# Performance work log

Measured on AMD Instinct MI355X. Metric: run time of the kernel, lower is better.

## Reference

```python
import jax, jax.numpy as jnp
import numpy as np

B, S, DIM = 2, 2048, 1024
H, W = 16, 256
HD = DIM // H
SCALE = HD ** -0.5


def setup_inputs() -> dict:
    key = jax.random.key(0)
    ks = jax.random.split(key, 9)
    std = DIM ** -0.5
    return {
        "x": jax.random.normal(ks[0], (B, S, DIM), dtype=jnp.float32),
        "Wq": jax.random.normal(ks[1], (DIM, DIM), dtype=jnp.float32) * std,
        "bq": jnp.zeros((DIM,), dtype=jnp.float32),
        "Wk": jax.random.normal(ks[2], (DIM, DIM), dtype=jnp.float32) * std,
        "bk": jnp.zeros((DIM,), dtype=jnp.float32),
        "Wv": jax.random.normal(ks[3], (DIM, DIM), dtype=jnp.float32) * std,
        "bv": jnp.zeros((DIM,), dtype=jnp.float32),
        "Wo": jax.random.normal(ks[4], (DIM, DIM), dtype=jnp.float32) * std,
        "bo": jnp.zeros((DIM,), dtype=jnp.float32),
    }


def reference(x, Wq, bq, Wk, bk, Wv, bv, Wo, bo):
    b, s, dim = x.shape
    q = (x @ Wq + bq).reshape(b, s, H, HD).transpose(0, 2, 1, 3)  # [B,H,S,HD]
    k = (x @ Wk + bk).reshape(b, s, H, HD).transpose(0, 2, 1, 3)
    v = (x @ Wv + bv).reshape(b, s, H, HD).transpose(0, 2, 1, 3)

    scores = jnp.einsum("bhid,bhjd->bhij", q, k) * SCALE  # [B,H,S,S]
    i = jnp.arange(s)[:, None]
    j = jnp.arange(s)[None, :]
    # valid keys: within causal sliding window [i-W+1, i]
    valid = (j <= i) & (j >= i - W + 1)
    scores = jnp.where(valid, scores, -jnp.inf)
    attn = jax.nn.softmax(scores, axis=-1)
    out = jnp.einsum("bhij,bhjd->bhid", attn, v)  # [B,H,S,HD]
    out = out.transpose(0, 2, 1, 3).reshape(b, s, dim)
    return out @ Wo + bo
```

## Files before the change

### kernel.cpp

```cpp
#include <hip/hip_runtime.h>
#include <stdint.h>

typedef __bf16 bf16;
typedef __bf16 bf16x8 __attribute__((ext_vector_type(8)));
typedef float f32x4 __attribute__((ext_vector_type(4)));

#define MFMA16(a, b, c) __builtin_amdgcn_mfma_f32_16x16x32_bf16((a), (b), (c), 0, 0, 0)

__device__ __forceinline__ void ldsdma16(const void* g, void* l) {
  __builtin_amdgcn_global_load_lds((const __attribute__((address_space(1))) void*)g,
                                   (__attribute__((address_space(3))) void*)l, 16, 0, 0);
}

__global__ __launch_bounds__(256) void prep_kernel(const float* __restrict__ x,
                                                   const float* __restrict__ Wq,
                                                   const float* __restrict__ Wk,
                                                   const float* __restrict__ Wv,
                                                   const float* __restrict__ Wo,
                                                   bf16* __restrict__ xb,
                                                   bf16* __restrict__ WT) {
  __shared__ float tile[64][65];
  if (blockIdx.z == 4) {
    const int t = (blockIdx.y * 16 + blockIdx.x) * 256 + threadIdx.x;
#pragma unroll
    for (int i = 0; i < 16; ++i) {
      const int idx = (t + i * 65536) * 4;
      float4 v = *(const float4*)(x + idx);
      union { bf16 h[4]; uint2 u; } p;
      p.h[0] = (bf16)v.x; p.h[1] = (bf16)v.y; p.h[2] = (bf16)v.z; p.h[3] = (bf16)v.w;
      *(uint2*)(xb + idx) = p.u;
    }
    return;
  }
  const float* src = blockIdx.z == 0 ? Wq : blockIdx.z == 1 ? Wk : blockIdx.z == 2 ? Wv : Wo;
  bf16* dst = WT + (size_t)blockIdx.z * 1024 * 1024;
  const int k0 = blockIdx.y * 64, n0 = blockIdx.x * 64;
  const int rr = threadIdx.x >> 6, c = threadIdx.x & 63;
#pragma unroll
  for (int i = 0; i < 16; ++i) {
    int r = i * 4 + rr;
    tile[r][c] = src[(size_t)(k0 + r) * 1024 + n0 + c];
  }
  __syncthreads();
#pragma unroll
  for (int i = 0; i < 16; ++i) {
    int r = i * 4 + rr;
    dst[(size_t)(n0 + r) * 1024 + k0 + c] = (bf16)tile[c][r];
  }
}

template <int NJ>
__device__ __forceinline__ void gemm_mainloop(const bf16* __restrict__ A,
                                              const bf16* __restrict__ BT, int K,
                                              int m0, int n0, bf16* As, bf16* Bs,
                                              f32x4 (&acc)[4][NJ]) {
  constexpr int BN = NJ * 32;
  const int tid = threadIdx.x;
  const int lane = tid & 63;
  const int wave = tid >> 6;
  const int wm = wave >> 1, wn = wave & 1;
  const int quad = lane >> 4, l16 = lane & 15;

  const f32x4 zero = {0.f, 0.f, 0.f, 0.f};
#pragma unroll
  for (int i = 0; i < 4; ++i)
#pragma unroll
    for (int j = 0; j < NJ; ++j) acc[i][j] = zero;

  for (int k0 = 0; k0 < K; k0 += 32) {
#pragma unroll
    for (int c = 0; c < 2; ++c) {
      int chunk = wave * 128 + c * 64 + lane;
      int row = chunk >> 2;
      int cg = (chunk & 3) ^ ((row >> 1) & 3);
      ldsdma16(A + (size_t)(m0 + row) * K + k0 + cg * 8,
               (char*)As + (size_t)(wave * 128 + c * 64) * 16);
    }
#pragma unroll
    for (int c = 0; c < BN / 64; ++c) {
      int chunk = wave * (BN / 64) * 64 + c * 64 + lane;
      int row = chunk >> 2;
      int cg = (chunk & 3) ^ ((row >> 1) & 3);
      ldsdma16(BT + (size_t)(n0 + row) * K + k0 + cg * 8,
               (char*)Bs + (size_t)(wave * (BN / 64) * 64 + c * 64) * 16);
    }
    __syncthreads();
    bf16x8 af[4], bfv[NJ];
#pragma unroll
    for (int i = 0; i < 4; ++i) {
      int ra = wm * 64 + i * 16 + l16;
      af[i] = ((const bf16x8*)As)[ra * 4 + (quad ^ ((ra >> 1) & 3))];
    }
#pragma unroll
    for (int j = 0; j < NJ; ++j) {
      int rb = wn * (BN / 2) + j * 16 + l16;
      bfv[j] = ((const bf16x8*)Bs)[rb * 4 + (quad ^ ((rb >> 1) & 3))];
    }
#pragma unroll
    for (int i = 0; i < 4; ++i)
#pragma unroll
      for (int j = 0; j < NJ; ++j) acc[i][j] = MFMA16(af[i], bfv[j], acc[i][j]);
    __syncthreads();
  }
}

__global__ __launch_bounds__(256) void qkv_gemm(const bf16* __restrict__ xb,
                                                const bf16* __restrict__ WT,
                                                const float* __restrict__ bq,
                                                const float* __restrict__ bk,
                                                const float* __restrict__ bv,
                                                bf16* __restrict__ Qd,
                                                bf16* __restrict__ Kd,
                                                bf16* __restrict__ Vd) {
  __shared__ bf16 As[128 * 32] __attribute__((aligned(16)));
  __shared__ bf16 Bs[128 * 32] __attribute__((aligned(16)));
  f32x4 acc[4][4];
  const int m0 = blockIdx.y * 128, n0 = blockIdx.x * 128;
  gemm_mainloop<4>(xb, WT, 1024, m0, n0, As, Bs, acc);

  const int lane = threadIdx.x & 63, wave = threadIdx.x >> 6;
  const int wm = wave >> 1, wn = wave & 1;
  const int quad = lane >> 4, l16 = lane & 15;
#pragma unroll
  for (int j = 0; j < 4; ++j) {
    const int n = n0 + wn * 64 + j * 16 + l16;
    const int sel = n >> 10, d = n & 1023;
    const float bias = (sel == 0 ? bq : sel == 1 ? bk : bv)[d];
    bf16* dst = (sel == 0 ? Qd : sel == 1 ? Kd : Vd);
    const float scl = (sel == 0) ? 0.125f : 1.f;
    const int h = d >> 6, hd = d & 63;
#pragma unroll
    for (int i = 0; i < 4; ++i) {
#pragma unroll
      for (int r = 0; r < 4; ++r) {
        const int token = m0 + wm * 64 + i * 16 + quad * 4 + r;
        const int bb = token >> 11, s = token & 2047;
        const float v = (acc[i][j][r] + bias) * scl;
        dst[((((size_t)bb * 16 + h) * 2048 + s) << 6) + hd] = (bf16)v;
      }
    }
  }
}

template <int NT, int MODE>
__device__ __forceinline__ void attn_phase(const int start, const bf16* __restrict__ Kb,
                                           const bf16* __restrict__ Vb, bf16* Ks, bf16* Vt,
                                           bf16* Psw, const bf16x8 qa0, const bf16x8 qa1,
                                           const int i0, float (&mrow)[4], float (&lrow)[4],
                                           f32x4 (&oacc)[4]) {
  const int tid = threadIdx.x, lane = tid & 63, wave = tid >> 6;
  const int quad = lane >> 4, l16 = lane & 15;
  const f32x4 zero = {0.f, 0.f, 0.f, 0.f};

  __syncthreads();
#pragma unroll
  for (int c = 0; c < NT / 2; ++c) {
    int chunk = c * 256 + wave * 64 + lane;
    int row = chunk >> 3;
    int cg = (chunk & 7) ^ (row & 7);
    ldsdma16(Kb + (size_t)(start + row) * 64 + cg * 8,
             (char*)Ks + (size_t)(c * 256 + wave * 64) * 16);
  }
  if (NT == 8) {
    const int key = tid >> 1, hc = (tid & 1) * 32;
    const bf16* vp = Vb + (size_t)(start + key) * 64 + hc;
    bf16x8 v0 = ((const bf16x8*)vp)[0], v1 = ((const bf16x8*)vp)[1];
    bf16x8 v2 = ((const bf16x8*)vp)[2], v3 = ((const bf16x8*)vp)[3];
#pragma unroll
    for (int i = 0; i < 8; ++i) Vt[(hc + i) * 136 + key] = v0[i];
#pragma unroll
    for (int i = 0; i < 8; ++i) Vt[(hc + 8 + i) * 136 + key] = v1[i];
#pragma unroll
    for (int i = 0; i < 8; ++i) Vt[(hc + 16 + i) * 136 + key] = v2[i];
#pragma unroll
    for (int i = 0; i < 8; ++i) Vt[(hc + 24 + i) * 136 + key] = v3[i];
  } else {
    const int key = tid >> 2, hc = (tid & 3) * 16;
    const bf16* vp = Vb + (size_t)(start + key) * 64 + hc;
    bf16x8 v0 = ((const bf16x8*)vp)[0], v1 = ((const bf16x8*)vp)[1];
#pragma unroll
    for (int i = 0; i < 8; ++i) Vt[(hc + i) * 136 + key] = v0[i];
#pragma unroll
    for (int i = 0; i < 8; ++i) Vt[(hc + 8 + i) * 136 + key] = v1[i];
  }
  __syncthreads();

  f32x4 sc[NT];
  __builtin_amdgcn_s_setprio(1);
#pragma unroll
  for (int nt = 0; nt < NT; ++nt) {
    int key = nt * 16 + l16;
    bf16x8 kb0 = ((const bf16x8*)Ks)[key * 8 + ((0 * 4 + quad) ^ (key & 7))];
    bf16x8 kb1 = ((const bf16x8*)Ks)[key * 8 + ((1 * 4 + quad) ^ (key & 7))];
    f32x4 s = zero;
    s = MFMA16(qa0, kb0, s);
    s = MFMA16(qa1, kb1, s);
    sc[nt] = s;
  }
  __builtin_amdgcn_s_setprio(0);

  float alpha[4];
#pragma unroll
  for (int r = 0; r < 4; ++r) {
    const int i = i0 + r;
    float mx = -1e30f;
#pragma unroll
    for (int nt = 0; nt < NT; ++nt) {
      float s = sc[nt][r];
      if (MODE == 1) {
        const bool valid = (start + nt * 16 + l16 + 255 >= i);
        s = valid ? s : -1e30f;
        sc[nt][r] = s;
      } else if (MODE == 2) {
        const bool valid = (start + nt * 16 + l16 <= i);
        s = valid ? s : -1e30f;
        sc[nt][r] = s;
      }
      mx = fmaxf(mx, s);
    }
#pragma unroll
    for (int m = 8; m >= 1; m >>= 1) mx = fmaxf(mx, __shfl_xor(mx, m, 64));
    const float mnew = fmaxf(mrow[r], mx);
    alpha[r] = __expf(mrow[r] - mnew);
    mrow[r] = mnew;
    float rs = 0.f;
#pragma unroll
    for (int nt = 0; nt < NT; ++nt) {
      const float p = __expf(sc[nt][r] - mnew);
      sc[nt][r] = p;
      rs += p;
    }
#pragma unroll
    for (int m = 8; m >= 1; m >>= 1) rs += __shfl_xor(rs, m, 64);
    lrow[r] = lrow[r] * alpha[r] + rs;
  }

#pragma unroll
  for (int nt = 0; nt < NT; ++nt)
#pragma unroll
    for (int r = 0; r < 4; ++r)
      Psw[(quad * 4 + r) * 136 + nt * 16 + l16] = (bf16)sc[nt][r];
  asm volatile("s_waitcnt lgkmcnt(0)" ::: "memory");
  bf16x8 pa[NT / 2];
#pragma unroll
  for (int ks = 0; ks < NT / 2; ++ks)
    pa[ks] = ((const bf16x8*)Psw)[l16 * 17 + ks * 4 + quad];

  __builtin_amdgcn_s_setprio(1);
#pragma unroll
  for (int ht = 0; ht < 4; ++ht) {
    f32x4 o = oacc[ht];
#pragma unroll
    for (int r = 0; r < 4; ++r) o[r] *= alpha[r];
#pragma unroll
    for (int ks = 0; ks < NT / 2; ++ks) {
      bf16x8 vb = ((const bf16x8*)Vt)[(ht * 16 + l16) * 17 + ks * 4 + quad];
      o = MFMA16(pa[ks], vb, o);
    }
    oacc[ht] = o;
  }
  __builtin_amdgcn_s_setprio(0);
}

__global__ __launch_bounds__(256) void attn_kernel(const bf16* __restrict__ Q,
                                                   const bf16* __restrict__ K,
                                                   const bf16* __restrict__ V,
                                                   bf16* __restrict__ Ao) {
  __shared__ bf16 Ks[128 * 64] __attribute__((aligned(16)));
  __shared__ bf16 Vt[64 * 136] __attribute__((aligned(16)));
  __shared__ bf16 Ps[4][16 * 136] __attribute__((aligned(16)));

  const int tid = threadIdx.x, lane = tid & 63, wave = tid >> 6;
  const int quad = lane >> 4, l16 = lane & 15;
  const int qt = blockIdx.x, h = blockIdx.y, b = blockIdx.z;
  const int q0 = qt * 64;
  const size_t base = ((size_t)(b * 16 + h)) * 2048 * 64;
  const bf16* Qb = Q + base + (size_t)q0 * 64;
  const bf16* Kb = K + base;
  const bf16* Vb = V + base;

  const bf16* qrow = Qb + (size_t)(wave * 16 + l16) * 64 + quad * 8;
  const bf16x8 qa0 = *(const bf16x8*)qrow;
  const bf16x8 qa1 = *(const bf16x8*)(qrow + 32);

  float mrow[4], lrow[4];
  f32x4 oacc[4];
  const f32x4 zero = {0.f, 0.f, 0.f, 0.f};
#pragma unroll
  for (int r = 0; r < 4; ++r) { mrow[r] = -1e30f; lrow[r] = 0.f; }
#pragma unroll
  for (int t = 0; t < 4; ++t) oacc[t] = zero;

  const int i0 = q0 + wave * 16 + quad * 4;
  bf16* Psw = Ps[wave];

  if (q0 >= 256)
    attn_phase<8, 1>(q0 - 256, Kb, Vb, Ks, Vt, Psw, qa0, qa1, i0, mrow, lrow, oacc);
  else if (q0 == 192)
    attn_phase<4, 0>(0, Kb, Vb, Ks, Vt, Psw, qa0, qa1, i0, mrow, lrow, oacc);
  if (q0 >= 128)
    attn_phase<8, 0>(q0 - 128, Kb, Vb, Ks, Vt, Psw, qa0, qa1, i0, mrow, lrow, oacc);
  else if (q0 == 64)
    attn_phase<4, 0>(0, Kb, Vb, Ks, Vt, Psw, qa0, qa1, i0, mrow, lrow, oacc);
  attn_phase<4, 2>(q0, Kb, Vb, Ks, Vt, Psw, qa0, qa1, i0, mrow, lrow, oacc);

#pragma unroll
  for (int r = 0; r < 4; ++r) {
    const float inv = 1.f / lrow[r];
    const int row = q0 + wave * 16 + quad * 4 + r;
    const size_t outb = ((size_t)(b * 2048 + row)) * 1024 + h * 64;
#pragma unroll
    for (int ht = 0; ht < 4; ++ht)
      Ao[outb + ht * 16 + l16] = (bf16)(oacc[ht][r] * inv);
  }
}

__global__ __launch_bounds__(256) void out_gemm(const bf16* __restrict__ Ain,
                                                const bf16* __restrict__ WoT,
                                                const float* __restrict__ bo,
                                                float* __restrict__ out) {
  __shared__ bf16 As[128 * 32] __attribute__((aligned(16)));
  __shared__ bf16 Bs[64 * 32] __attribute__((aligned(16)));
  f32x4 acc[4][2];
  const int m0 = blockIdx.y * 128, n0 = blockIdx.x * 64;
  gemm_mainloop<2>(Ain, WoT, 1024, m0, n0, As, Bs, acc);

  const int lane = threadIdx.x & 63, wave = threadIdx.x >> 6;
  const int wm = wave >> 1, wn = wave & 1;
  const int quad = lane >> 4, l16 = lane & 15;
#pragma unroll
  for (int j = 0; j < 2; ++j) {
    const int n = n0 + wn * 32 + j * 16 + l16;
    const float bias = bo[n];
#pragma unroll
    for (int i = 0; i < 4; ++i) {
#pragma unroll
      for (int r = 0; r < 4; ++r) {
        const int token = m0 + wm * 64 + i * 16 + quad * 4 + r;
        out[(size_t)token * 1024 + n] = acc[i][j][r] + bias;
      }
    }
  }
}

extern "C" void kernel_launch(void* const* d_in, const int* in_sizes, int n_in,
                              void* d_out, int out_size, void* d_ws, size_t ws_size,
                              hipStream_t stream) {
  const float* x  = (const float*)d_in[0];
  const float* Wq = (const float*)d_in[1];
  const float* bq = (const float*)d_in[2];
  const float* Wk = (const float*)d_in[3];
  const float* bk = (const float*)d_in[4];
  const float* Wv = (const float*)d_in[5];
  const float* bv = (const float*)d_in[6];
  const float* Wo = (const float*)d_in[7];
  const float* bo = (const float*)d_in[8];
  float* out = (float*)d_out;

  char* ws = (char*)d_ws;
  bf16* xb = (bf16*)(ws);
  bf16* WT = (bf16*)(ws + ((size_t)8 << 20));
  bf16* Qd = (bf16*)(ws + ((size_t)16 << 20));
  bf16* Kd = (bf16*)(ws + ((size_t)24 << 20));
  bf16* Vd = (bf16*)(ws + ((size_t)32 << 20));
  bf16* Ao = (bf16*)(ws + ((size_t)40 << 20));

  prep_kernel<<<dim3(16, 16, 5), 256, 0, stream>>>(x, Wq, Wk, Wv, Wo, xb, WT);
  qkv_gemm<<<dim3(24, 32), 256, 0, stream>>>(xb, WT, bq, bk, bv, Qd, Kd, Vd);
  attn_kernel<<<dim3(32, 16, 2), 256, 0, stream>>>(Qd, Kd, Vd, Ao);
  out_gemm<<<dim3(16, 32), 256, 0, stream>>>(Ao, WT + (size_t)3 * 1024 * 1024, bo, out);
}
```

Before: 168.3 us.

## Replace QKV GEMM with 256x256 eight-wave pipelined kernel using LDS DMA

```diff
diff --git a/kernel.cpp b/kernel.cpp
--- a/kernel.cpp
+++ b/kernel.cpp
@@ -47,6 +47,160 @@
     int r = i * 4 + rr;
     dst[(size_t)(n0 + r) * 1024 + k0 + c] = (bf16)tile[c][r];
   }
+}
+
+__device__ __forceinline__ void stage_half(const bf16* __restrict__ src, int rowbase,
+                                           int koff, char* lds, int bufq, int wave,
+                                           int lane) {
+#pragma unroll
+  for (int i = 0; i < 2; ++i) {
+    int chunk = i * 512 + wave * 64 + lane;
+    int row = chunk >> 3;
+    int cg = (chunk & 7) ^ (row & 7);
+    ldsdma16(src + (size_t)(rowbase + row) * 1024 + koff + cg * 8,
+             lds + bufq * 16384 + (i * 512 + wave * 64) * 16);
+  }
+}
+
+__device__ __forceinline__ void ld_frag4(const bf16* lds, int bufq, int rbase, int quad,
+                                         int l16, bf16x8 (&d)[4][2]) {
+  const bf16x8* hb = (const bf16x8*)lds + bufq * 1024;
+#pragma unroll
+  for (int mf = 0; mf < 4; ++mf) {
+    int row = rbase + mf * 16 + l16;
+#pragma unroll
+    for (int kk = 0; kk < 2; ++kk)
+      d[mf][kk] = hb[row * 8 + ((kk * 4 + quad) ^ (row & 7))];
+  }
+}
+
+__device__ __forceinline__ void ld_frag2(const bf16* lds, int bufq, int rbase, int quad,
+                                         int l16, bf16x8 (&d)[2][2]) {
+  const bf16x8* hb = (const bf16x8*)lds + bufq * 1024;
+#pragma unroll
+  for (int nf = 0; nf < 2; ++nf) {
+    int row = rbase + nf * 16 + l16;
+#pragma unroll
+    for (int kk = 0; kk < 2; ++kk)
+      d[nf][kk] = hb[row * 8 + ((kk * 4 + quad) ^ (row & 7))];
+  }
+}
+
+template <int MQ, int NQ>
+__device__ __forceinline__ void mma_quad(f32x4 (&acc)[8][4], const bf16x8 (&a)[4][2],
+                                         const bf16x8 (&b)[2][2]) {
+  __builtin_amdgcn_s_setprio(1);
+#pragma unroll
+  for (int mf = 0; mf < 4; ++mf)
+#pragma unroll
+    for (int nf = 0; nf < 2; ++nf)
+#pragma unroll
+      for (int kk = 0; kk < 2; ++kk)
+        acc[MQ * 4 + mf][NQ * 2 + nf] =
+            MFMA16(a[mf][kk], b[nf][kk], acc[MQ * 4 + mf][NQ * 2 + nf]);
+  __builtin_amdgcn_s_setprio(0);
+}
+
+#define QBAR1() { __builtin_amdgcn_s_barrier(); \
+                  asm volatile("s_waitcnt lgkmcnt(0)" ::: "memory"); }
+#define QBAR2() { __builtin_amdgcn_s_barrier(); }
+
+template <bool PRE>
+__device__ __forceinline__ void qkv_iter(int k0, const bf16* __restrict__ xb,
+                                         const bf16* __restrict__ BT, int m0, int n0,
+                                         bf16* As, bf16* Bs, f32x4 (&acc)[8][4], int wave,
+                                         int lane, int wm, int wn, int quad, int l16) {
+  bf16x8 aF[4][2], b0F[2][2], b1F[2][2];
+  ld_frag4(As, 0, wm * 64, quad, l16, aF);
+  ld_frag2(Bs, 0, wn * 32, quad, l16, b0F);
+  stage_half(xb, m0 + 128, k0 + 64, (char*)As, 3, wave, lane);
+  QBAR1(); mma_quad<0, 0>(acc, aF, b0F); QBAR2();
+  ld_frag2(Bs, 1, wn * 32, quad, l16, b1F);
+  stage_half(BT, n0, k0 + 64, (char*)Bs, 2, wave, lane);
+  QBAR1(); mma_quad<0, 1>(acc, aF, b1F); QBAR2();
+  ld_frag4(As, 1, wm * 64, quad, l16, aF);
+  if (PRE) stage_half(xb, m0, k0 + 128, (char*)As, 0, wave, lane);
+  QBAR1(); mma_quad<1, 1>(acc, aF, b1F); QBAR2();
+  if (PRE) stage_half(BT, n0 + 128, k0 + 128, (char*)Bs, 1, wave, lane);
+  QBAR1(); mma_quad<1, 0>(acc, aF, b0F);
+  if (PRE) { asm volatile("s_waitcnt vmcnt(4)" ::: "memory"); }
+  else     { asm volatile("s_waitcnt vmcnt(0)" ::: "memory"); }
+  QBAR2();
+  ld_frag4(As, 2, wm * 64, quad, l16, aF);
+  ld_frag2(Bs, 2, wn * 32, quad, l16, b0F);
+  if (PRE) stage_half(xb, m0 + 128, k0 + 128, (char*)As, 1, wave, lane);
+  QBAR1(); mma_quad<0, 0>(acc, aF, b0F); QBAR2();
+  ld_frag2(Bs, 3, wn * 32, quad, l16, b1F);
+  if (PRE) stage_half(BT, n0, k0 + 128, (char*)Bs, 0, wave, lane);
+  QBAR1(); mma_quad<0, 1>(acc, aF, b1F); QBAR2();
+  ld_frag4(As, 3, wm * 64, quad, l16, aF);
+  if (PRE) stage_half(xb, m0, k0 + 192, (char*)As, 2, wave, lane);
+  QBAR1(); mma_quad<1, 1>(acc, aF, b1F); QBAR2();
+  if (PRE) stage_half(BT, n0 + 128, k0 + 192, (char*)Bs, 3, wave, lane);
+  QBAR1(); mma_quad<1, 0>(acc, aF, b0F);
+  if (PRE) { asm volatile("s_waitcnt vmcnt(4)" ::: "memory"); }
+  QBAR2();
+}
+
+__global__ __launch_bounds__(512, 2) void qkv_gemm8(const bf16* __restrict__ xb,
+                                                    const bf16* __restrict__ WT,
+                                                    const float* __restrict__ bq,
+                                                    const float* __restrict__ bk,
+                                                    const float* __restrict__ bv,
+                                                    bf16* __restrict__ Qd,
+                                                    bf16* __restrict__ Kd,
+                                                    bf16* __restrict__ Vd) {
+  extern __shared__ char smem_raw[];
+  bf16* As = (bf16*)smem_raw;
+  bf16* Bs = (bf16*)(smem_raw + 65536);
+
+  const int tid = threadIdx.x, lane = tid & 63, wave = tid >> 6;
+  const int wm = wave >> 2, wn = wave & 3;
+  const int quad = lane >> 4, l16 = lane & 15;
+  const int m0 = blockIdx.y * 256, n0 = blockIdx.x * 256;
+
+  f32x4 acc[8][4];
+  const f32x4 zero = {0.f, 0.f, 0.f, 0.f};
+#pragma unroll
+  for (int i = 0; i < 8; ++i)
+#pragma unroll
+    for (int j = 0; j < 4; ++j) acc[i][j] = zero;
+
+  stage_half(xb, m0, 0, (char*)As, 0, wave, lane);
+  stage_half(WT, n0, 0, (char*)Bs, 0, wave, lane);
+  stage_half(xb, m0 + 128, 0, (char*)As, 1, wave, lane);
+  stage_half(WT, n0 + 128, 0, (char*)Bs, 1, wave, lane);
+  stage_half(xb, m0, 64, (char*)As, 2, wave, lane);
+  stage_half(WT, n0 + 128, 64, (char*)Bs, 3, wave, lane);
+  asm volatile("s_waitcnt vmcnt(4)" ::: "memory");
+  __builtin_amdgcn_s_barrier();
+
+  for (int j = 0; j < 7; ++j)
+    qkv_iter<true>(j * 128, xb, WT, m0, n0, As, Bs, acc, wave, lane, wm, wn, quad, l16);
+  qkv_iter<false>(896, xb, WT, m0, n0, As, Bs, acc, wave, lane, wm, wn, quad, l16);
+
+#pragma unroll
+  for (int MQ = 0; MQ < 2; ++MQ)
+#pragma unroll
+    for (int mf = 0; mf < 4; ++mf)
+#pragma unroll
+      for (int NQ = 0; NQ < 2; ++NQ)
+#pragma unroll
+        for (int nf = 0; nf < 2; ++nf) {
+          const int n = n0 + NQ * 128 + wn * 32 + nf * 16 + l16;
+          const int sel = n >> 10, d = n & 1023;
+          const float bias = (sel == 0 ? bq : sel == 1 ? bk : bv)[d];
+          bf16* dst = (sel == 0 ? Qd : sel == 1 ? Kd : Vd);
+          const float scl = (sel == 0) ? 0.125f : 1.f;
+          const int h = d >> 6, hd = d & 63;
+#pragma unroll
+          for (int r = 0; r < 4; ++r) {
+            const int token = m0 + MQ * 128 + wm * 64 + mf * 16 + quad * 4 + r;
+            const int bb = token >> 11, s = token & 2047;
+            const float v = (acc[MQ * 4 + mf][NQ * 2 + nf][r] + bias) * scl;
+            dst[((((size_t)bb * 16 + h) * 2048 + s) << 6) + hd] = (bf16)v;
+          }
+        }
 }
 
 template <int NJ>
@@ -101,44 +255,6 @@
 #pragma unroll
       for (int j = 0; j < NJ; ++j) acc[i][j] = MFMA16(af[i], bfv[j], acc[i][j]);
     __syncthreads();
-  }
-}
-
-__global__ __launch_bounds__(256) void qkv_gemm(const bf16* __restrict__ xb,
-                                                const bf16* __restrict__ WT,
-                                                const float* __restrict__ bq,
-                                                const float* __restrict__ bk,
-                                                const float* __restrict__ bv,
-                                                bf16* __restrict__ Qd,
-                                                bf16* __restrict__ Kd,
-                                                bf16* __restrict__ Vd) {
-  __shared__ bf16 As[128 * 32] __attribute__((aligned(16)));
-  __shared__ bf16 Bs[128 * 32] __attribute__((aligned(16)));
-  f32x4 acc[4][4];
-  const int m0 = blockIdx.y * 128, n0 = blockIdx.x * 128;
-  gemm_mainloop<4>(xb, WT, 1024, m0, n0, As, Bs, acc);
-
-  const int lane = threadIdx.x & 63, wave = threadIdx.x >> 6;
-  const int wm = wave >> 1, wn = wave & 1;
-  const int quad = lane >> 4, l16 = lane & 15;
-#pragma unroll
-  for (int j = 0; j < 4; ++j) {
-    const int n = n0 + wn * 64 + j * 16 + l16;
-    const int sel = n >> 10, d = n & 1023;
-    const float bias = (sel == 0 ? bq : sel == 1 ? bk : bv)[d];
-    bf16* dst = (sel == 0 ? Qd : sel == 1 ? Kd : Vd);
-    const float scl = (sel == 0) ? 0.125f : 1.f;
-    const int h = d >> 6, hd = d & 63;
-#pragma unroll
-    for (int i = 0; i < 4; ++i) {
-#pragma unroll
-      for (int r = 0; r < 4; ++r) {
-        const int token = m0 + wm * 64 + i * 16 + quad * 4 + r;
-        const int bb = token >> 11, s = token & 2047;
-        const float v = (acc[i][j][r] + bias) * scl;
-        dst[((((size_t)bb * 16 + h) * 2048 + s) << 6) + hd] = (bf16)v;
-      }
-    }
   }
 }
 
@@ -365,8 +481,11 @@
   bf16* Vd = (bf16*)(ws + ((size_t)32 << 20));
   bf16* Ao = (bf16*)(ws + ((size_t)40 << 20));
 
+  (void)hipFuncSetAttribute((const void*)qkv_gemm8,
+                            hipFuncAttributeMaxDynamicSharedMemorySize, 131072);
+
   prep_kernel<<<dim3(16, 16, 5), 256, 0, stream>>>(x, Wq, Wk, Wv, Wo, xb, WT);
-  qkv_gemm<<<dim3(24, 32), 256, 0, stream>>>(xb, WT, bq, bk, bv, Qd, Kd, Vd);
+  qkv_gemm8<<<dim3(12, 16), 512, 131072, stream>>>(xb, WT, bq, bk, bv, Qd, Kd, Vd);
   attn_kernel<<<dim3(32, 16, 2), 256, 0, stream>>>(Qd, Kd, Vd, Ao);
   out_gemm<<<dim3(16, 32), 256, 0, stream>>>(Ao, WT + (size_t)3 * 1024 * 1024, bo, out);
 }
```

Result: no change. 169.1 us (+0.5%).

## Double-buffer V staging in attention, load K directly, pipeline out-projection GEMM

Applied to the files above, without the earlier changes.

```diff
diff --git a/kernel.cpp b/kernel.cpp
--- a/kernel.cpp
+++ b/kernel.cpp
@@ -49,12 +49,10 @@
   }
 }
 
-template <int NJ>
-__device__ __forceinline__ void gemm_mainloop(const bf16* __restrict__ A,
-                                              const bf16* __restrict__ BT, int K,
-                                              int m0, int n0, bf16* As, bf16* Bs,
-                                              f32x4 (&acc)[4][NJ]) {
-  constexpr int BN = NJ * 32;
+__device__ __forceinline__ void gemm_mainloop4(const bf16* __restrict__ A,
+                                               const bf16* __restrict__ BT, int K,
+                                               int m0, int n0, bf16* As, bf16* Bs,
+                                               f32x4 (&acc)[4][4]) {
   const int tid = threadIdx.x;
   const int lane = tid & 63;
   const int wave = tid >> 6;
@@ -65,41 +63,33 @@
 #pragma unroll
   for (int i = 0; i < 4; ++i)
 #pragma unroll
-    for (int j = 0; j < NJ; ++j) acc[i][j] = zero;
-
+    for (int j = 0; j < 4; ++j) acc[i][j] = zero;
+
+  const int ch0 = wave * 128 + lane;
   for (int k0 = 0; k0 < K; k0 += 32) {
 #pragma unroll
     for (int c = 0; c < 2; ++c) {
-      int chunk = wave * 128 + c * 64 + lane;
+      int chunk = ch0 + c * 64;
       int row = chunk >> 2;
       int cg = (chunk & 3) ^ ((row >> 1) & 3);
       ldsdma16(A + (size_t)(m0 + row) * K + k0 + cg * 8,
                (char*)As + (size_t)(wave * 128 + c * 64) * 16);
-    }
-#pragma unroll
-    for (int c = 0; c < BN / 64; ++c) {
-      int chunk = wave * (BN / 64) * 64 + c * 64 + lane;
-      int row = chunk >> 2;
-      int cg = (chunk & 3) ^ ((row >> 1) & 3);
       ldsdma16(BT + (size_t)(n0 + row) * K + k0 + cg * 8,
-               (char*)Bs + (size_t)(wave * (BN / 64) * 64 + c * 64) * 16);
+               (char*)Bs + (size_t)(wave * 128 + c * 64) * 16);
     }
     __syncthreads();
-    bf16x8 af[4], bfv[NJ];
+    bf16x8 af[4], bfv[4];
 #pragma unroll
     for (int i = 0; i < 4; ++i) {
       int ra = wm * 64 + i * 16 + l16;
       af[i] = ((const bf16x8*)As)[ra * 4 + (quad ^ ((ra >> 1) & 3))];
-    }
-#pragma unroll
-    for (int j = 0; j < NJ; ++j) {
-      int rb = wn * (BN / 2) + j * 16 + l16;
-      bfv[j] = ((const bf16x8*)Bs)[rb * 4 + (quad ^ ((rb >> 1) & 3))];
+      int rb = wn * 64 + i * 16 + l16;
+      bfv[i] = ((const bf16x8*)Bs)[rb * 4 + (quad ^ ((rb >> 1) & 3))];
     }
 #pragma unroll
     for (int i = 0; i < 4; ++i)
 #pragma unroll
-      for (int j = 0; j < NJ; ++j) acc[i][j] = MFMA16(af[i], bfv[j], acc[i][j]);
+      for (int j = 0; j < 4; ++j) acc[i][j] = MFMA16(af[i], bfv[j], acc[i][j]);
     __syncthreads();
   }
 }
@@ -116,7 +106,7 @@
   __shared__ bf16 Bs[128 * 32] __attribute__((aligned(16)));
   f32x4 acc[4][4];
   const int m0 = blockIdx.y * 128, n0 = blockIdx.x * 128;
-  gemm_mainloop<4>(xb, WT, 1024, m0, n0, As, Bs, acc);
+  gemm_mainloop4(xb, WT, 1024, m0, n0, As, Bs, acc);
 
   const int lane = threadIdx.x & 63, wave = threadIdx.x >> 6;
   const int wm = wave >> 1, wn = wave & 1;
@@ -142,62 +132,65 @@
   }
 }
 
-template <int NT, int MODE>
-__device__ __forceinline__ void attn_phase(const int start, const bf16* __restrict__ Kb,
-                                           const bf16* __restrict__ Vb, bf16* Ks, bf16* Vt,
-                                           bf16* Psw, const bf16x8 qa0, const bf16x8 qa1,
-                                           const int i0, float (&mrow)[4], float (&lrow)[4],
+template <int NT>
+__device__ __forceinline__ void loadv(const bf16* __restrict__ Vb, int start,
+                                      bf16x8 (&vp)[4]) {
+  const int tid = threadIdx.x;
+  if (NT == 8) {
+    const int key = tid >> 1, hc = (tid & 1) * 32;
+    const bf16x8* p = (const bf16x8*)(Vb + (size_t)(start + key) * 64 + hc);
+#pragma unroll
+    for (int r = 0; r < 4; ++r) vp[r] = p[r];
+  } else {
+    const int key = tid >> 2, hc = (tid & 3) * 16;
+    const bf16x8* p = (const bf16x8*)(Vb + (size_t)(start + key) * 64 + hc);
+#pragma unroll
+    for (int r = 0; r < 2; ++r) vp[r] = p[r];
+  }
+}
+
+template <int NT, int MODE, int NNT>
+__device__ __forceinline__ void attn_phase(int start, int nstart,
+                                           const bf16* __restrict__ Kb,
+                                           const bf16* __restrict__ Vb, bf16* Vtc,
+                                           bf16* Psw, bf16x8 (&vp)[4], bf16x8 (&vn)[4],
+                                           const bf16x8 qa0, const bf16x8 qa1, int i0,
+                                           float (&mrow)[4], float (&lrow)[4],
                                            f32x4 (&oacc)[4]) {
-  const int tid = threadIdx.x, lane = tid & 63, wave = tid >> 6;
+  const int tid = threadIdx.x, lane = tid & 63;
   const int quad = lane >> 4, l16 = lane & 15;
   const f32x4 zero = {0.f, 0.f, 0.f, 0.f};
 
-  __syncthreads();
-#pragma unroll
-  for (int c = 0; c < NT / 2; ++c) {
-    int chunk = c * 256 + wave * 64 + lane;
-    int row = chunk >> 3;
-    int cg = (chunk & 7) ^ (row & 7);
-    ldsdma16(Kb + (size_t)(start + row) * 64 + cg * 8,
-             (char*)Ks + (size_t)(c * 256 + wave * 64) * 16);
-  }
   if (NT == 8) {
     const int key = tid >> 1, hc = (tid & 1) * 32;
-    const bf16* vp = Vb + (size_t)(start + key) * 64 + hc;
-    bf16x8 v0 = ((const bf16x8*)vp)[0], v1 = ((const bf16x8*)vp)[1];
-    bf16x8 v2 = ((const bf16x8*)vp)[2], v3 = ((const bf16x8*)vp)[3];
-#pragma unroll
-    for (int i = 0; i < 8; ++i) Vt[(hc + i) * 136 + key] = v0[i];
-#pragma unroll
-    for (int i = 0; i < 8; ++i) Vt[(hc + 8 + i) * 136 + key] = v1[i];
-#pragma unroll
-    for (int i = 0; i < 8; ++i) Vt[(hc + 16 + i) * 136 + key] = v2[i];
-#pragma unroll
-    for (int i = 0; i < 8; ++i) Vt[(hc + 24 + i) * 136 + key] = v3[i];
+#pragma unroll
+    for (int r2 = 0; r2 < 4; ++r2)
+#pragma unroll
+      for (int i = 0; i < 8; ++i) Vtc[(hc + r2 * 8 + i) * 136 + key] = vp[r2][i];
   } else {
     const int key = tid >> 2, hc = (tid & 3) * 16;
-    const bf16* vp = Vb + (size_t)(start + key) * 64 + hc;
-    bf16x8 v0 = ((const bf16x8*)vp)[0], v1 = ((const bf16x8*)vp)[1];
-#pragma unroll
-    for (int i = 0; i < 8; ++i) Vt[(hc + i) * 136 + key] = v0[i];
-#pragma unroll
-    for (int i = 0; i < 8; ++i) Vt[(hc + 8 + i) * 136 + key] = v1[i];
-  }
-  __syncthreads();
+#pragma unroll
+    for (int r2 = 0; r2 < 2; ++r2)
+#pragma unroll
+      for (int i = 0; i < 8; ++i) Vtc[(hc + r2 * 8 + i) * 136 + key] = vp[r2][i];
+  }
+  if (NNT > 0) loadv<NNT>(Vb, nstart, vn);
+
+  asm volatile("s_waitcnt lgkmcnt(0)" ::: "memory");
+  __builtin_amdgcn_s_barrier();
 
   f32x4 sc[NT];
-  __builtin_amdgcn_s_setprio(1);
 #pragma unroll
   for (int nt = 0; nt < NT; ++nt) {
-    int key = nt * 16 + l16;
-    bf16x8 kb0 = ((const bf16x8*)Ks)[key * 8 + ((0 * 4 + quad) ^ (key & 7))];
-    bf16x8 kb1 = ((const bf16x8*)Ks)[key * 8 + ((1 * 4 + quad) ^ (key & 7))];
+    const int key = nt * 16 + l16;
+    const bf16* kp = Kb + (size_t)(start + key) * 64 + quad * 8;
+    const bf16x8 kb0 = *(const bf16x8*)kp;
+    const bf16x8 kb1 = *(const bf16x8*)(kp + 32);
     f32x4 s = zero;
     s = MFMA16(qa0, kb0, s);
     s = MFMA16(qa1, kb1, s);
     sc[nt] = s;
   }
-  __builtin_amdgcn_s_setprio(0);
 
   float alpha[4];
 #pragma unroll
@@ -254,7 +247,7 @@
     for (int r = 0; r < 4; ++r) o[r] *= alpha[r];
 #pragma unroll
     for (int ks = 0; ks < NT / 2; ++ks) {
-      bf16x8 vb = ((const bf16x8*)Vt)[(ht * 16 + l16) * 17 + ks * 4 + quad];
+      bf16x8 vb = ((const bf16x8*)Vtc)[(ht * 16 + l16) * 17 + ks * 4 + quad];
       o = MFMA16(pa[ks], vb, o);
     }
     oacc[ht] = o;
@@ -266,8 +259,7 @@
                                                    const bf16* __restrict__ K,
                                                    const bf16* __restrict__ V,
                                                    bf16* __restrict__ Ao) {
-  __shared__ bf16 Ks[128 * 64] __attribute__((aligned(16)));
-  __shared__ bf16 Vt[64 * 136] __attribute__((aligned(16)));
+  __shared__ bf16 Vt[2][64 * 136] __attribute__((aligned(16)));
   __shared__ bf16 Ps[4][16 * 136] __attribute__((aligned(16)));
 
   const int tid = threadIdx.x, lane = tid & 63, wave = tid >> 6;
@@ -293,16 +285,30 @@
 
   const int i0 = q0 + wave * 16 + quad * 4;
   bf16* Psw = Ps[wave];
-
-  if (q0 >= 256)
-    attn_phase<8, 1>(q0 - 256, Kb, Vb, Ks, Vt, Psw, qa0, qa1, i0, mrow, lrow, oacc);
-  else if (q0 == 192)
-    attn_phase<4, 0>(0, Kb, Vb, Ks, Vt, Psw, qa0, qa1, i0, mrow, lrow, oacc);
-  if (q0 >= 128)
-    attn_phase<8, 0>(q0 - 128, Kb, Vb, Ks, Vt, Psw, qa0, qa1, i0, mrow, lrow, oacc);
-  else if (q0 == 64)
-    attn_phase<4, 0>(0, Kb, Vb, Ks, Vt, Psw, qa0, qa1, i0, mrow, lrow, oacc);
-  attn_phase<4, 2>(q0, Kb, Vb, Ks, Vt, Psw, qa0, qa1, i0, mrow, lrow, oacc);
+  bf16x8 vpA[4], vpB[4];
+
+  if (qt >= 4) {
+    loadv<8>(Vb, q0 - 256, vpA);
+    attn_phase<8, 1, 8>(q0 - 256, q0 - 128, Kb, Vb, Vt[0], Psw, vpA, vpB, qa0, qa1, i0, mrow, lrow, oacc);
+    attn_phase<8, 0, 4>(q0 - 128, q0, Kb, Vb, Vt[1], Psw, vpB, vpA, qa0, qa1, i0, mrow, lrow, oacc);
+    attn_phase<4, 2, 0>(q0, 0, Kb, Vb, Vt[0], Psw, vpA, vpB, qa0, qa1, i0, mrow, lrow, oacc);
+  } else if (qt == 3) {
+    loadv<4>(Vb, 0, vpA);
+    attn_phase<4, 0, 8>(0, 64, Kb, Vb, Vt[0], Psw, vpA, vpB, qa0, qa1, i0, mrow, lrow, oacc);
+    attn_phase<8, 0, 4>(64, 192, Kb, Vb, Vt[1], Psw, vpB, vpA, qa0, qa1, i0, mrow, lrow, oacc);
+    attn_phase<4, 2, 0>(192, 0, Kb, Vb, Vt[0], Psw, vpA, vpB, qa0, qa1, i0, mrow, lrow, oacc);
+  } else if (qt == 2) {
+    loadv<8>(Vb, 0, vpA);
+    attn_phase<8, 0, 4>(0, 128, Kb, Vb, Vt[0], Psw, vpA, vpB, qa0, qa1, i0, mrow, lrow, oacc);
+    attn_phase<4, 2, 0>(128, 0, Kb, Vb, Vt[1], Psw, vpB, vpA, qa0, qa1, i0, mrow, lrow, oacc);
+  } else if (qt == 1) {
+    loadv<4>(Vb, 0, vpA);
+    attn_phase<4, 0, 4>(0, 64, Kb, Vb, Vt[0], Psw, vpA, vpB, qa0, qa1, i0, mrow, lrow, oacc);
+    attn_phase<4, 2, 0>(64, 0, Kb, Vb, Vt[1], Psw, vpB, vpA, qa0, qa1, i0, mrow, lrow, oacc);
+  } else {
+    loadv<4>(Vb, 0, vpA);
+    attn_phase<4, 2, 0>(0, 0, Kb, Vb, Vt[0], Psw, vpA, vpB, qa0, qa1, i0, mrow, lrow, oacc);
+  }
 
 #pragma unroll
   for (int r = 0; r < 4; ++r) {
@@ -319,15 +325,77 @@
                                                 const bf16* __restrict__ WoT,
                                                 const float* __restrict__ bo,
                                                 float* __restrict__ out) {
-  __shared__ bf16 As[128 * 32] __attribute__((aligned(16)));
-  __shared__ bf16 Bs[64 * 32] __attribute__((aligned(16)));
-  f32x4 acc[4][2];
-  const int m0 = blockIdx.y * 128, n0 = blockIdx.x * 64;
-  gemm_mainloop<2>(Ain, WoT, 1024, m0, n0, As, Bs, acc);
-
-  const int lane = threadIdx.x & 63, wave = threadIdx.x >> 6;
+  __shared__ bf16 As[2][128 * 64] __attribute__((aligned(16)));
+  __shared__ bf16 Bs[2][64 * 64] __attribute__((aligned(16)));
+  const int tid = threadIdx.x, lane = tid & 63, wave = tid >> 6;
   const int wm = wave >> 1, wn = wave & 1;
   const int quad = lane >> 4, l16 = lane & 15;
+  const int m0 = blockIdx.y * 128, n0 = blockIdx.x * 64;
+
+  f32x4 acc[4][2];
+  const f32x4 zero = {0.f, 0.f, 0.f, 0.f};
+#pragma unroll
+  for (int i = 0; i < 4; ++i)
+#pragma unroll
+    for (int j = 0; j < 2; ++j) acc[i][j] = zero;
+
+#define OUT_STAGE(t)                                                                \
+  {                                                                                 \
+    const int _buf = (t) & 1;                                                       \
+    const int _k0 = (t) * 64;                                                       \
+    _Pragma("unroll")                                                               \
+    for (int _i = 0; _i < 4; ++_i) {                                                \
+      const int chunk = _i * 256 + tid;                                             \
+      const int row = chunk >> 3, cg = (chunk & 7) ^ (row & 7);                     \
+      ldsdma16(Ain + (size_t)(m0 + row) * 1024 + _k0 + cg * 8,                      \
+               (char*)As[_buf] + (size_t)(_i * 256 + wave * 64) * 16);              \
+    }                                                                               \
+    _Pragma("unroll")                                                               \
+    for (int _i = 0; _i < 2; ++_i) {                                                \
+      const int chunk = _i * 256 + tid;                                             \
+      const int row = chunk >> 3, cg = (chunk & 7) ^ (row & 7);                     \
+      ldsdma16(WoT + (size_t)(n0 + row) * 1024 + _k0 + cg * 8,                      \
+               (char*)Bs[_buf] + (size_t)(_i * 256 + wave * 64) * 16);              \
+    }                                                                               \
+  }
+
+  OUT_STAGE(0);
+  for (int t = 0; t < 16; ++t) {
+    if (t < 15) {
+      OUT_STAGE(t + 1);
+      asm volatile("s_waitcnt vmcnt(6)" ::: "memory");
+    } else {
+      asm volatile("s_waitcnt vmcnt(0)" ::: "memory");
+    }
+    __builtin_amdgcn_s_barrier();
+    bf16x8 aF[4][2], bF[2][2];
+    const bf16x8* ha = (const bf16x8*)As[t & 1];
+#pragma unroll
+    for (int mf = 0; mf < 4; ++mf) {
+      const int row = wm * 64 + mf * 16 + l16;
+      aF[mf][0] = ha[row * 8 + (quad ^ (row & 7))];
+      aF[mf][1] = ha[row * 8 + ((4 + quad) ^ (row & 7))];
+    }
+    const bf16x8* hb = (const bf16x8*)Bs[t & 1];
+#pragma unroll
+    for (int nf = 0; nf < 2; ++nf) {
+      const int row = wn * 32 + nf * 16 + l16;
+      bF[nf][0] = hb[row * 8 + (quad ^ (row & 7))];
+      bF[nf][1] = hb[row * 8 + ((4 + quad) ^ (row & 7))];
+    }
+    __builtin_amdgcn_s_setprio(1);
+#pragma unroll
+    for (int mf = 0; mf < 4; ++mf)
+#pragma unroll
+      for (int nf = 0; nf < 2; ++nf)
+#pragma unroll
+        for (int kk = 0; kk < 2; ++kk)
+          acc[mf][nf] = MFMA16(aF[mf][kk], bF[nf][kk], acc[mf][nf]);
+    __builtin_amdgcn_s_setprio(0);
+    __builtin_amdgcn_s_barrier();
+  }
+#undef OUT_STAGE
+
 #pragma unroll
   for (int j = 0; j < 2; ++j) {
     const int n = n0 + wn * 32 + j * 16 + l16;
```

Measured after the change: 176.2 us. +4.7%, slower.
